# Kernel optimization log

Hardware: AMD Instinct MI355X
Metric: run time of the kernel (lower is better)

The kernel has to match this reference:

```python
import jax, jax.numpy as jnp
import numpy as np
from jax import lax

N, L, D = 16, 512, 256
FILT, K = 256, 3
MAXDUR = 8
MEL_MAX = L * (MAXDUR - 1)  # 3584, worst-case sum of durations
LN_EPS = 1e-5


def _conv1d(x, w, b):
    # x: [N, L, Cin], w: [K, Cin, Cout] -> [N, L, Cout], SAME padding (pad=(K-1)//2)
    return lax.conv_general_dilated(x, w, (1,), 'SAME',
                                    dimension_numbers=('NWC', 'WIO', 'NWC')) + b


def _layer_norm(x, g, b):
    mu = jnp.mean(x, axis=-1, keepdims=True)
    var = jnp.var(x, axis=-1, keepdims=True)
    return (x - mu) * lax.rsqrt(var + LN_EPS) * g + b


def _variance_predictor(x, conv1_w, conv1_b, ln1_g, ln1_b,
                        conv2_w, conv2_b, ln2_g, ln2_b, lin_w, lin_b):
    # Standard FastSpeech duration predictor (dropout omitted: eval mode)
    h = _layer_norm(jax.nn.relu(_conv1d(x, conv1_w, conv1_b)), ln1_g, ln1_b)
    h = _layer_norm(jax.nn.relu(_conv1d(h, conv2_w, conv2_b)), ln2_g, ln2_b)
    return (h @ lin_w + lin_b)[..., 0]  # [N, L] log-durations


def setup_inputs() -> dict:
    key = jax.random.key(0)
    ks = jax.random.split(key, 6)
    s = 0.02
    return {
        'x': jax.random.normal(ks[0], (N, L, D), jnp.float32),
        'conv1_w': jax.random.normal(ks[1], (K, D, FILT), jnp.float32) * s,
        'conv1_b': jnp.zeros((FILT,), jnp.float32),
        'ln1_g': jnp.ones((FILT,), jnp.float32),
        'ln1_b': jnp.zeros((FILT,), jnp.float32),
        'conv2_w': jax.random.normal(ks[2], (K, FILT, FILT), jnp.float32) * s,
        'conv2_b': jnp.zeros((FILT,), jnp.float32),
        'ln2_g': jnp.ones((FILT,), jnp.float32),
        'ln2_b': jnp.zeros((FILT,), jnp.float32),
        'lin_w': jax.random.normal(ks[3], (FILT, 1), jnp.float32) * s,
        'lin_b': jnp.zeros((1,), jnp.float32),
        'target': jax.random.randint(ks[4], (N, L), 0, MAXDUR, jnp.int32),
        'mel_max_length': MEL_MAX,
    }


def reference(x, conv1_w, conv1_b, ln1_g, ln1_b, conv2_w, conv2_b,
              ln2_g, ln2_b, lin_w, lin_b, target, mel_max_length):
    log_dur = _variance_predictor(x, conv1_w, conv1_b, ln1_g, ln1_b,
                                  conv2_w, conv2_b, ln2_g, ln2_b, lin_w, lin_b)
    # Dense alignment (faithful to create_alignment), padded directly to mel_max_length
    M = mel_max_length  # static python int
    end = jnp.cumsum(target, axis=1)            # [N, L]
    start = end - target                        # [N, L]
    idx = jnp.arange(M, dtype=target.dtype)[None, :, None]  # [1, M, 1]
    align = ((idx >= start[:, None, :]) & (idx < end[:, None, :])).astype(x.dtype)  # [N, M, L]
    output = jnp.einsum('nml,nld->nmd', align, x)  # [N, M, D]
    return output, log_dur
```

## Files before the change

### kernel.cpp

```cpp
#include <hip/hip_runtime.h>
#include <cstddef>

#define N_ 16
#define L_ 512
#define D_ 256
#define M_ 3584
#define LN_EPS 1e-5f

typedef __attribute__((ext_vector_type(8))) short bf16x8;
typedef __attribute__((ext_vector_type(4))) float f32x4;

__device__ inline unsigned int f2bf_raw(float f) {
    union { float f; unsigned int u; } v; v.f = f;
    return (v.u + 0x7FFFu + ((v.u >> 16) & 1u)) >> 16;
}
__device__ inline unsigned int pack2bf(float lo, float hi) {
    return f2bf_raw(lo) | (f2bf_raw(hi) << 16);
}
__device__ inline float bf2f(unsigned int hw) {
    union { unsigned int u; float f; } v; v.u = hw << 16; return v.f;
}
__device__ inline int aswz(int row, int colb) {
    return row * 512 + (((colb & 0x1F0) ^ ((row & 7) << 4)) | (colb & 0xF));
}

__global__ __launch_bounds__(512)
void prep_kernel(const float* __restrict__ W1, unsigned short* __restrict__ Wt1,
                 const float* __restrict__ W2, unsigned short* __restrict__ Wt2,
                 const int* __restrict__ target, int* __restrict__ idx) {
    __shared__ union { float t[2][32][33]; int s[L_]; } sm;
    const int bid = blockIdx.x;
    if (bid < 192) {
        const int half = threadIdx.x >> 8, st = threadIdx.x & 255;
        const int tile = bid * 2 + half;
        const int kb = (tile % 24) * 32;
        const int cb = ((tile / 24) % 8) * 32;
        const float* W = (tile >= 192) ? W2 : W1;
        unsigned short* Wt = (tile >= 192) ? Wt2 : Wt1;
        const int tx = st & 31, ty = st >> 5;
#pragma unroll
        for (int r = 0; r < 32; r += 8)
            sm.t[half][ty + r][tx] = W[(size_t)(kb + ty + r) * 256 + cb + tx];
        __syncthreads();
        const int jl = st >> 7, l = (st >> 1) & 63, e0 = (st & 1) * 4;
        ushort4 o;
        o.x = (unsigned short)f2bf_raw(sm.t[half][(l >> 4) * 8 + e0 + 0][jl * 16 + (l & 15)]);
        o.y = (unsigned short)f2bf_raw(sm.t[half][(l >> 4) * 8 + e0 + 1][jl * 16 + (l & 15)]);
        o.z = (unsigned short)f2bf_raw(sm.t[half][(l >> 4) * 8 + e0 + 2][jl * 16 + (l & 15)]);
        o.w = (unsigned short)f2bf_raw(sm.t[half][(l >> 4) * 8 + e0 + 3][jl * 16 + (l & 15)]);
        *(ushort4*)(Wt + ((((size_t)(kb >> 5) * 16) + (cb >> 4) + jl) * 64 + l) * 8 + e0) = o;
    } else {
        const int n = bid - 192, t = threadIdx.x;
        const int tv = target[n * L_ + t];
        sm.s[t] = tv;
        __syncthreads();
        for (int off = 1; off < L_; off <<= 1) {
            int v = (t >= off) ? sm.s[t - off] : 0;
            __syncthreads();
            sm.s[t] += v;
            __syncthreads();
        }
        const int e = sm.s[t], st0 = e - tv;
        const int total = sm.s[L_ - 1];
        int* row = idx + (size_t)n * M_;
        for (int j = st0; j < e; ++j) row[j] = t;
        for (int m = total + t; m < M_; m += 512) row[m] = -1;
    }
}

template <int NR, int MAXS>
__device__ __forceinline__ void conv_phase(const unsigned char* Ab,
        const unsigned short* __restrict__ Wf,
        int wv, int lane, int fr, int fg, f32x4 (&acc)[NR]) {
    const unsigned short* wb = Wf + ((size_t)wv * 64 + lane) * 8;
    uint4 p0 = *(const uint4*)(wb);
    uint4 p1 = *(const uint4*)(wb + 8192);
    for (int ks = 0; ks < 24; ++ks) {
        uint4 q;
        if (ks < 22) q = *(const uint4*)(wb + (size_t)(ks + 2) * 8192);
        const int cib = (ks & 7) * 64 + fg * 16;
        const int koff = ks >> 3;
        bf16x8 av[NR];
#pragma unroll
        for (int r = 0; r < NR; ++r) {
            int ar = r * 16 + fr + koff;
            if (ar > MAXS) ar = MAXS;
            av[r] = *(const bf16x8*)(Ab + ar * 512 + (cib ^ ((ar & 7) << 4)));
        }
        bf16x8 bb = *(bf16x8*)&p0;
        __builtin_amdgcn_s_setprio(1);
#pragma unroll
        for (int r = 0; r < NR; ++r)
            acc[r] = __builtin_amdgcn_mfma_f32_16x16x32_bf16(bb, av[r], acc[r], 0, 0, 0);
        __builtin_amdgcn_s_setprio(0);
        p0 = p1; p1 = q;
    }
}

template <int NR, int NROWS>
__device__ __forceinline__ void store_h(unsigned char* Ab, f32x4 (&acc)[NR],
        const float* __restrict__ bias, int wv, int fr, int fg) {
    const int co = wv * 16 + fg * 4;
    const float4 bb = *(const float4*)&bias[co];
#pragma unroll
    for (int r = 0; r < NR; ++r) {
        const int slot = r * 16 + fr;
        if (slot < NROWS) {
            uint2 o;
            o.x = pack2bf(fmaxf(acc[r][0] + bb.x, 0.f), fmaxf(acc[r][1] + bb.y, 0.f));
            o.y = pack2bf(fmaxf(acc[r][2] + bb.z, 0.f), fmaxf(acc[r][3] + bb.w, 0.f));
            *(uint2*)(Ab + aswz(slot, 2 * co)) = o;
        }
    }
}

__global__ __launch_bounds__(1024, 4)
void mega_kernel(const float* __restrict__ x,
                 const unsigned short* __restrict__ Wf1,
                 const unsigned short* __restrict__ Wf2,
                 const float* __restrict__ b1, const float* __restrict__ g1,
                 const float* __restrict__ be1,
                 const float* __restrict__ b2, const float* __restrict__ g2,
                 const float* __restrict__ be2,
                 const float* __restrict__ lw, const float* __restrict__ lb,
                 const int* __restrict__ idx,
                 float* __restrict__ out0, float* __restrict__ log_dur) {
    __shared__ unsigned char smA[36 * 512];
    const int tid = threadIdx.x, lane = tid & 63, wv = tid >> 6;
    const int bid = blockIdx.x;
    const int row0 = bid * 32;
    const int n = row0 >> 9, l0 = row0 & 511;
    const int fr = lane & 15, fg = lane >> 4;

    {
        const int m0 = (bid & 15) * 224 + wv;
        const int* ip = idx + (size_t)n * M_ + m0;
        const float* xn = x + (size_t)n * L_ * D_ + lane * 4;
        float* op = out0 + ((size_t)n * M_ + m0) * D_ + lane * 4;
#pragma unroll
        for (int i = 0; i < 14; ++i) {
            const int li = ip[i * 16];
            f32x4 o = {0.f, 0.f, 0.f, 0.f};
            if (li >= 0) o = *(const f32x4*)(xn + (size_t)li * D_);
            __builtin_nontemporal_store(o, (f32x4*)(op + (size_t)i * 16 * D_));
        }
    }

    for (int i = tid; i < 36 * 64; i += 1024) {
        int r = i >> 6, c4 = i & 63;
        int l = l0 - 2 + r;
        float4 v = {0.f, 0.f, 0.f, 0.f};
        if (l >= 0 && l < L_)
            v = ((const float4*)(x + ((size_t)(n * L_ + l)) * D_))[c4];
        uint2 p;
        p.x = pack2bf(v.x, v.y);
        p.y = pack2bf(v.z, v.w);
        *(uint2*)(smA + aswz(r, c4 * 8)) = p;
    }
    __syncthreads();

    f32x4 a1[3];
#pragma unroll
    for (int r = 0; r < 3; ++r) a1[r] = (f32x4){0.f, 0.f, 0.f, 0.f};
    conv_phase<3, 35>(smA, Wf1, wv, lane, fr, fg, a1);
    __syncthreads();
    store_h<3, 34>(smA, a1, b1, wv, fr, fg);
    __syncthreads();

    {
        const float4 gv = *(const float4*)&g1[lane * 4];
        const float4 bv = *(const float4*)&be1[lane * 4];
        for (int mm = wv; mm < 34; mm += 16) {
            const int addr = aswz(mm, lane * 8);
            const int hrow = l0 - 1 + mm;
            if (hrow < 0 || hrow >= L_) {
                *(uint2*)(smA + addr) = (uint2){0u, 0u};
                continue;
            }
            uint2 pv = *(uint2*)(smA + addr);
            float v0 = bf2f(pv.x & 0xFFFFu), v1 = bf2f(pv.x >> 16);
            float v2 = bf2f(pv.y & 0xFFFFu), v3 = bf2f(pv.y >> 16);
            float s = v0 + v1 + v2 + v3;
            float ss = v0 * v0 + v1 * v1 + v2 * v2 + v3 * v3;
#pragma unroll
            for (int off = 32; off; off >>= 1) {
                s += __shfl_xor(s, off);
                ss += __shfl_xor(ss, off);
            }
            const float mu = s * (1.f / D_);
            const float var = ss * (1.f / D_) - mu * mu;
            const float rs = rsqrtf(var + LN_EPS);
            uint2 o;
            o.x = pack2bf((v0 - mu) * rs * gv.x + bv.x, (v1 - mu) * rs * gv.y + bv.y);
            o.y = pack2bf((v2 - mu) * rs * gv.z + bv.z, (v3 - mu) * rs * gv.w + bv.w);
            *(uint2*)(smA + addr) = o;
        }
    }
    __syncthreads();

    f32x4 a2[2];
#pragma unroll
    for (int r = 0; r < 2; ++r) a2[r] = (f32x4){0.f, 0.f, 0.f, 0.f};
    conv_phase<2, 33>(smA, Wf2, wv, lane, fr, fg, a2);
    __syncthreads();
    store_h<2, 32>(smA, a2, b2, wv, fr, fg);
    __syncthreads();

    {
        const float4 gv = *(const float4*)&g2[lane * 4];
        const float4 bv = *(const float4*)&be2[lane * 4];
        const float4 wvv = *(const float4*)&lw[lane * 4];
        for (int mm = wv; mm < 32; mm += 16) {
            uint2 pv = *(uint2*)(smA + aswz(mm, lane * 8));
            float v0 = bf2f(pv.x & 0xFFFFu), v1 = bf2f(pv.x >> 16);
            float v2 = bf2f(pv.y & 0xFFFFu), v3 = bf2f(pv.y >> 16);
            float s = v0 + v1 + v2 + v3;
            float ss = v0 * v0 + v1 * v1 + v2 * v2 + v3 * v3;
#pragma unroll
            for (int off = 32; off; off >>= 1) {
                s += __shfl_xor(s, off);
                ss += __shfl_xor(ss, off);
            }
            const float mu = s * (1.f / D_);
            const float var = ss * (1.f / D_) - mu * mu;
            const float rs = rsqrtf(var + LN_EPS);
            float dot = ((v0 - mu) * rs * gv.x + bv.x) * wvv.x
                      + ((v1 - mu) * rs * gv.y + bv.y) * wvv.y
                      + ((v2 - mu) * rs * gv.z + bv.z) * wvv.z
                      + ((v3 - mu) * rs * gv.w + bv.w) * wvv.w;
#pragma unroll
            for (int off = 32; off; off >>= 1) dot += __shfl_xor(dot, off);
            if (lane == 0) log_dur[row0 + mm] = dot + lb[0];
        }
    }
}

extern "C" void kernel_launch(void* const* d_in, const int* in_sizes, int n_in,
                              void* d_out, int out_size, void* d_ws, size_t ws_size,
                              hipStream_t stream) {
    const float* x   = (const float*)d_in[0];
    const float* w1  = (const float*)d_in[1];
    const float* b1  = (const float*)d_in[2];
    const float* g1  = (const float*)d_in[3];
    const float* be1 = (const float*)d_in[4];
    const float* w2  = (const float*)d_in[5];
    const float* b2  = (const float*)d_in[6];
    const float* g2  = (const float*)d_in[7];
    const float* be2 = (const float*)d_in[8];
    const float* lw  = (const float*)d_in[9];
    const float* lb  = (const float*)d_in[10];
    const int* target = (const int*)d_in[11];

    float* out0 = (float*)d_out;
    float* log_dur = out0 + (size_t)N_ * M_ * D_;

    unsigned short* w1f = (unsigned short*)d_ws;
    unsigned short* w2f = w1f + 24 * 8192;
    int* idx = (int*)(w2f + 24 * 8192);

    prep_kernel<<<208, 512, 0, stream>>>(w1, w1f, w2, w2f, target, idx);
    mega_kernel<<<256, 1024, 0, stream>>>(x, w1f, w2f, b1, g1, be1,
                                          b2, g2, be2, lw, lb, idx,
                                          out0, log_dur);
}
```

Baseline: 35.95 us.

## Interleave alignment gather-stores into conv MFMA loops to overlap memory traffic

The alignment gather/scatter of output rows no longer runs as a separate phase before the convolutions. It is now spread across the two conv loops: 12 rows are interleaved into the conv1 K-loop and 2 into the conv2 K-loop, with one row loaded ahead of each store. The aim is to hide the global memory traffic of the large output write behind MFMA compute. In exchange it adds register pressure from the li array and gcur, fully unrolls the loops, and risks the stores stalling the MFMA pipeline.

```diff
diff --git a/kernel.cpp b/kernel.cpp
--- a/kernel.cpp
+++ b/kernel.cpp
@@ -68,35 +68,6 @@
     }
 }
 
-template <int NR, int MAXS>
-__device__ __forceinline__ void conv_phase(const unsigned char* Ab,
-        const unsigned short* __restrict__ Wf,
-        int wv, int lane, int fr, int fg, f32x4 (&acc)[NR]) {
-    const unsigned short* wb = Wf + ((size_t)wv * 64 + lane) * 8;
-    uint4 p0 = *(const uint4*)(wb);
-    uint4 p1 = *(const uint4*)(wb + 8192);
-    for (int ks = 0; ks < 24; ++ks) {
-        uint4 q;
-        if (ks < 22) q = *(const uint4*)(wb + (size_t)(ks + 2) * 8192);
-        const int cib = (ks & 7) * 64 + fg * 16;
-        const int koff = ks >> 3;
-        bf16x8 av[NR];
-#pragma unroll
-        for (int r = 0; r < NR; ++r) {
-            int ar = r * 16 + fr + koff;
-            if (ar > MAXS) ar = MAXS;
-            av[r] = *(const bf16x8*)(Ab + ar * 512 + (cib ^ ((ar & 7) << 4)));
-        }
-        bf16x8 bb = *(bf16x8*)&p0;
-        __builtin_amdgcn_s_setprio(1);
-#pragma unroll
-        for (int r = 0; r < NR; ++r)
-            acc[r] = __builtin_amdgcn_mfma_f32_16x16x32_bf16(bb, av[r], acc[r], 0, 0, 0);
-        __builtin_amdgcn_s_setprio(0);
-        p0 = p1; p1 = q;
-    }
-}
-
 template <int NR, int NROWS>
 __device__ __forceinline__ void store_h(unsigned char* Ab, f32x4 (&acc)[NR],
         const float* __restrict__ bias, int wv, int fr, int fg) {
@@ -132,19 +103,13 @@
     const int n = row0 >> 9, l0 = row0 & 511;
     const int fr = lane & 15, fg = lane >> 4;
 
-    {
-        const int m0 = (bid & 15) * 224 + wv;
-        const int* ip = idx + (size_t)n * M_ + m0;
-        const float* xn = x + (size_t)n * L_ * D_ + lane * 4;
-        float* op = out0 + ((size_t)n * M_ + m0) * D_ + lane * 4;
-#pragma unroll
-        for (int i = 0; i < 14; ++i) {
-            const int li = ip[i * 16];
-            f32x4 o = {0.f, 0.f, 0.f, 0.f};
-            if (li >= 0) o = *(const f32x4*)(xn + (size_t)li * D_);
-            __builtin_nontemporal_store(o, (f32x4*)(op + (size_t)i * 16 * D_));
-        }
-    }
+    const int m0 = (bid & 15) * 224 + wv;
+    const int* ip = idx + (size_t)n * M_ + m0;
+    const float* xn = x + (size_t)n * L_ * D_ + lane * 4;
+    float* op = out0 + ((size_t)n * M_ + m0) * D_ + lane * 4;
+    int li[14];
+#pragma unroll
+    for (int i = 0; i < 14; ++i) li[i] = ip[i * 16];
 
     for (int i = tid; i < 36 * 64; i += 1024) {
         int r = i >> 6, c4 = i & 63;
@@ -162,7 +127,43 @@
     f32x4 a1[3];
 #pragma unroll
     for (int r = 0; r < 3; ++r) a1[r] = (f32x4){0.f, 0.f, 0.f, 0.f};
-    conv_phase<3, 35>(smA, Wf1, wv, lane, fr, fg, a1);
+    {
+        const unsigned short* wb = Wf1 + ((size_t)wv * 64 + lane) * 8;
+        uint4 p0 = *(const uint4*)(wb);
+        uint4 p1 = *(const uint4*)(wb + 8192);
+        f32x4 gcur = {0.f, 0.f, 0.f, 0.f};
+        if (li[0] >= 0) gcur = *(const f32x4*)(xn + (size_t)li[0] * D_);
+#pragma unroll
+        for (int ks = 0; ks < 24; ++ks) {
+            uint4 q;
+            if (ks < 22) q = *(const uint4*)(wb + (size_t)(ks + 2) * 8192);
+            const int cib = (ks & 7) * 64 + fg * 16;
+            const int koff = ks >> 3;
+            bf16x8 av[3];
+#pragma unroll
+            for (int r = 0; r < 3; ++r) {
+                int ar = r * 16 + fr + koff;
+                if (ar > 35) ar = 35;
+                av[r] = *(const bf16x8*)(smA + ar * 512 + (cib ^ ((ar & 7) << 4)));
+            }
+            bf16x8 bb = *(bf16x8*)&p0;
+            __builtin_amdgcn_s_setprio(1);
+#pragma unroll
+            for (int r = 0; r < 3; ++r)
+                a1[r] = __builtin_amdgcn_mfma_f32_16x16x32_bf16(bb, av[r], a1[r], 0, 0, 0);
+            __builtin_amdgcn_s_setprio(0);
+            if (ks & 1) {
+                const int g = ks >> 1;
+                __builtin_nontemporal_store(gcur, (f32x4*)(op + (size_t)g * 16 * D_));
+                if (g + 1 < 12) {
+                    gcur = (f32x4){0.f, 0.f, 0.f, 0.f};
+                    if (li[g + 1] >= 0)
+                        gcur = *(const f32x4*)(xn + (size_t)li[g + 1] * D_);
+                }
+            }
+            p0 = p1; p1 = q;
+        }
+    }
     __syncthreads();
     store_h<3, 34>(smA, a1, b1, wv, fr, fg);
     __syncthreads();
@@ -201,7 +202,42 @@
     f32x4 a2[2];
 #pragma unroll
     for (int r = 0; r < 2; ++r) a2[r] = (f32x4){0.f, 0.f, 0.f, 0.f};
-    conv_phase<2, 33>(smA, Wf2, wv, lane, fr, fg, a2);
+    {
+        const unsigned short* wb = Wf2 + ((size_t)wv * 64 + lane) * 8;
+        uint4 p0 = *(const uint4*)(wb);
+        uint4 p1 = *(const uint4*)(wb + 8192);
+        f32x4 gcur = {0.f, 0.f, 0.f, 0.f};
+        if (li[12] >= 0) gcur = *(const f32x4*)(xn + (size_t)li[12] * D_);
+#pragma unroll
+        for (int ks = 0; ks < 24; ++ks) {
+            uint4 q;
+            if (ks < 22) q = *(const uint4*)(wb + (size_t)(ks + 2) * 8192);
+            const int cib = (ks & 7) * 64 + fg * 16;
+            const int koff = ks >> 3;
+            bf16x8 av[2];
+#pragma unroll
+            for (int r = 0; r < 2; ++r) {
+                int ar = r * 16 + fr + koff;
+                if (ar > 33) ar = 33;
+                av[r] = *(const bf16x8*)(smA + ar * 512 + (cib ^ ((ar & 7) << 4)));
+            }
+            bf16x8 bb = *(bf16x8*)&p0;
+            __builtin_amdgcn_s_setprio(1);
+#pragma unroll
+            for (int r = 0; r < 2; ++r)
+                a2[r] = __builtin_amdgcn_mfma_f32_16x16x32_bf16(bb, av[r], a2[r], 0, 0, 0);
+            __builtin_amdgcn_s_setprio(0);
+            if (ks == 5) {
+                __builtin_nontemporal_store(gcur, (f32x4*)(op + (size_t)12 * 16 * D_));
+                gcur = (f32x4){0.f, 0.f, 0.f, 0.f};
+                if (li[13] >= 0) gcur = *(const f32x4*)(xn + (size_t)li[13] * D_);
+            }
+            if (ks == 17) {
+                __builtin_nontemporal_store(gcur, (f32x4*)(op + (size_t)13 * 16 * D_));
+            }
+            p0 = p1; p1 = q;
+        }
+    }
     __syncthreads();
     store_h<2, 32>(smA, a2, b2, wv, fr, fg);
     __syncthreads();
```

Result: faster. 31.10 us (-13.5%).
